# Optimization experiments

Measured on AMD Instinct MI355X. Metric: run time of the kernel, lower is better.

The kernel has to match this reference:

```python
import jax, jax.numpy as jnp
import numpy as np

EPS = 1e-6  # nn.PairwiseDistance default eps (added to the difference)


def setup_inputs() -> dict:
    key = jax.random.key(0)
    feature = jax.random.normal(key, (16384, 256), dtype=jnp.float32)
    return {"feature": feature}


def reference(feature) -> jnp.ndarray:
    n = feature.shape[0]
    # all-pairs inner products [n, n]
    dots = jnp.matmul(feature, feature.T)
    # mask self-similarity on the diagonal with -1 (as in the torch code)
    dots = dots.at[jnp.diag_indices(n)].set(-1.0)
    # row-wise nearest neighbor (argmax of inner product)
    I = jnp.argmax(dots, axis=1)  # [n] int
    # PairwiseDistance(p=2): ||x1 - x2 + eps||_2
    diff = feature - feature[I] + EPS  # [n, d]
    distances = jnp.sqrt(jnp.sum(diff * diff, axis=1))  # [n]
    loss_uniform = -jnp.mean(jnp.log(n * distances))
    return loss_uniform
```

## Files before the change

kernel.cpp:

```cpp
#include <hip/hip_runtime.h>
#include <hip/hip_bf16.h>
#include <math.h>


#define NROWS 16384
#define DIM   256
#define EPSF  1e-6f

typedef __attribute__((ext_vector_type(4))) float f32x4;

typedef const __attribute__((address_space(1))) void* gas1_t;
typedef __attribute__((address_space(3))) void* las3_t;

__device__ __forceinline__ void glds16(const void* g, void* l) {
    __builtin_amdgcn_global_load_lds((gas1_t)g, (las3_t)l, 16, 0, 0);
}

__device__ __forceinline__ unsigned umax2(unsigned a, unsigned b) {
    return a > b ? a : b;
}

__device__ __forceinline__ unsigned f2e4m3(float f) {
    union { float f; unsigned u; } x; x.f = f;
    const unsigned s = (x.u >> 24) & 0x80u;
    const unsigned au = x.u & 0x7FFFFFFFu;
    const float af = __uint_as_float(au);
    if (au < 0x3C800000u) {
        const int q = (int)(af * 512.0f + 0.5f);
        return s | (unsigned)q;
    }
    const unsigned add = 0x7FFFFu + ((au >> 20) & 1u);
    const unsigned v = au + add;
    const unsigned e = (v >> 23) - 120u;
    return s | (e << 3) | ((v >> 20) & 7u);
}

__global__ __launch_bounds__(256)
void convert_kernel(const float* __restrict__ F, unsigned char* __restrict__ F8,
                    unsigned long long* __restrict__ packed)
{
    const int t = blockIdx.x * 256 + threadIdx.x;
    const float4 a = *reinterpret_cast<const float4*>(F + (size_t)t * 8);
    const float4 b = *reinterpret_cast<const float4*>(F + (size_t)t * 8 + 4);
    const unsigned lo = f2e4m3(a.x) | (f2e4m3(a.y) << 8) |
                        (f2e4m3(a.z) << 16) | (f2e4m3(a.w) << 24);
    const unsigned hi = f2e4m3(b.x) | (f2e4m3(b.y) << 8) |
                        (f2e4m3(b.z) << 16) | (f2e4m3(b.w) << 24);
    uint2 v; v.x = lo; v.y = hi;
    *reinterpret_cast<uint2*>(F8 + (size_t)t * 8) = v;
    if (t < NROWS) packed[t] = 0ull;
}

__global__ __launch_bounds__(256, 3)
void mfma_sym_fp8_pipe(const unsigned char* __restrict__ F8,
                       unsigned long long* __restrict__ packed,
                       unsigned long long* __restrict__ scratch)
{
    __shared__ __align__(16) unsigned char As[32768];
    __shared__ __align__(16) unsigned char Bs[16384];
    __shared__ unsigned cmb[256];

    const int tid = threadIdx.x;
    const int w   = tid >> 6;
    const int l   = tid & 63;

    const int bid  = (int)blockIdx.x;
    const int kgen = bid >> 8;
    const int m5   = (bid >> 3) & 31;
    const int ck   = bid & 7;
    const int rs   = (kgen == 0) ? m5 :
                     (kgen == 1) ? 63 - m5 :
                     (kgen == 2) ? 64 + m5 : 127 - m5;
    const int span = 128 - rs;
    const int t0   = rs + ((span * ck) >> 3);
    const int t1   = rs + ((span * (ck + 1)) >> 3);
    if (t0 >= t1) return;

    const int row0 = rs * 128;
    const int wrow = (w >> 1) * 64;
    const int wcol = (w & 1) * 64;
    const int lc   = l & 15;
    const int lr4  = l >> 4;
    const int k16r = lr4 >> 1;
    const int odd  = lr4 & 1;

    #pragma unroll
    for (int m = 0; m < 8; ++m) {
        const int q = 8 * w + m;
        glds16(F8 + (size_t)(row0 + (q & 1) * 64 + l) * DIM + (q >> 1) * 16,
               &As[q * 1024]);
    }
    #pragma unroll
    for (int sl = 0; sl < 3; ++sl)
        glds16(F8 + (size_t)(t0 * 128 + (w & 1) * 64 + l) * DIM + sl * 32 + (w >> 1) * 16,
               &Bs[sl * 4096 + w * 1024]);

    const long* __restrict__ Al = reinterpret_cast<const long*>(As);

    f32x4 acc[4][4];
    #pragma unroll
    for (int i = 0; i < 4; ++i)
        #pragma unroll
        for (int j = 0; j < 4; ++j)
            acc[i][j] = (f32x4){512.f, 512.f, 512.f, 512.f};

    unsigned best[4][4] = {};

    for (int t = t0; t < t1; ++t) {
        const bool dt   = (t == rs);
        const bool last = (t == t1 - 1);

        #pragma unroll
        for (int q = 0; q < 8; ++q) {
            if (!last || q < 6)      asm volatile("s_waitcnt vmcnt(2)" ::: "memory");
            else if (q == 6)         asm volatile("s_waitcnt vmcnt(1)" ::: "memory");
            else                     asm volatile("s_waitcnt vmcnt(0)" ::: "memory");
            __builtin_amdgcn_s_barrier();

            if (!last || q < 5) {
                const int nt = t + ((q + 3) >> 3);
                const int nq = (q + 3) & 7;
                glds16(F8 + (size_t)(nt * 128 + (w & 1) * 64 + l) * DIM
                           + nq * 32 + (w >> 1) * 16,
                       &Bs[((q + 3) & 3) * 4096 + w * 1024]);
            }

            const long* __restrict__ Bl =
                reinterpret_cast<const long*>(Bs + (q & 3) * 4096);

            long afv[4], bfv[4];
            #pragma unroll
            for (int i = 0; i < 4; ++i)
                afv[i] = Al[(2 * q + k16r) * 256 + (wrow + i * 16 + lc) * 2 + odd];
            #pragma unroll
            for (int j = 0; j < 4; ++j)
                bfv[j] = Bl[k16r * 256 + (wcol + j * 16 + lc) * 2 + odd];
            #pragma unroll
            for (int j = 0; j < 4; ++j)
                #pragma unroll
                for (int i = 0; i < 4; ++i)
                    acc[i][j] = __builtin_amdgcn_mfma_f32_16x16x32_fp8_fp8(
                        afv[i], bfv[j], acc[i][j], 0, 0, 0);
        }

        const int tl = t - t0;
        unsigned cbA[4];
        #pragma unroll
        for (int j = 0; j < 4; ++j)
            cbA[j] = 2047u - (unsigned)(tl * 128 + wcol + j * 16 + lc);

        #pragma unroll
        for (int j = 0; j < 4; ++j) {
            unsigned kb = 0u;
            #pragma unroll
            for (int i = 0; i < 4; ++i)
                #pragma unroll
                for (int g = 0; g < 4; ++g) {
                    const int r_loc = wrow + i * 16 + lr4 * 4 + g;
                    unsigned m = __float_as_uint(acc[i][j][g]) & 0xFFFFF800u;
                    if (dt && (wcol + j * 16 + lc == r_loc)) m = 0u;
                    best[i][g] = umax2(best[i][g], m | cbA[j]);
                    kb = umax2(kb, m | (unsigned)(127 - r_loc));
                    acc[i][j][g] = 512.f;
                }
            kb = umax2(kb, (unsigned)__shfl_xor((int)kb, 16));
            kb = umax2(kb, (unsigned)__shfl_xor((int)kb, 32));
            if (lr4 == 0) cmb[(w >> 1) * 128 + wcol + j * 16 + lc] = kb;
        }
        asm volatile("s_waitcnt lgkmcnt(0)" ::: "memory");
        __builtin_amdgcn_s_barrier();
        if (w < 2) {
            const int c = w * 64 + l;
            const unsigned km = umax2(cmb[c], cmb[128 + c]);
            const unsigned grow = (unsigned)row0 + (127u - (km & 0x7FFu));
            scratch[((size_t)t * 128 + rs) * 128 + c] =
                ((unsigned long long)(km & 0xFFFFF800u) << 32) |
                (0xFFFFFFFFu - grow);
        }
    }

    #pragma unroll
    for (int i = 0; i < 4; ++i)
        #pragma unroll
        for (int g = 0; g < 4; ++g) {
            unsigned key = best[i][g];
            #pragma unroll
            for (int m = 8; m >= 1; m >>= 1)
                key = umax2(key, (unsigned)__shfl_xor((int)key, m));
            if (lc == 0) {
                const int r = row0 + wrow + i * 16 + lr4 * 4 + g;
                const unsigned c = (unsigned)(t0 * 128) + (2047u - (key & 0x7FFu));
                atomicMax(&packed[r],
                          ((unsigned long long)(key & 0xFFFFF800u) << 32) |
                          (0xFFFFFFFFu - c));
            }
        }
}

__global__ __launch_bounds__(256)
void dist_loss_kernel(const float* __restrict__ F,
                      const unsigned long long* __restrict__ packed,
                      const unsigned long long* __restrict__ scratch,
                      double* __restrict__ partials)
{
    const int tid  = threadIdx.x;
    const int lane = tid & 63;
    const int w    = tid >> 6;
    const int gw   = blockIdx.x * 4 + w;
    double local = 0.0;
    for (int r = gw; r < NROWS; r += 1024) {
        const int tR = r >> 7;
        const int cl = r & 127;
        unsigned long long best = packed[r];
        const unsigned long long* base = scratch + (size_t)tR * 16384 + cl;
        if (lane <= tR) {
            unsigned long long v = base[(size_t)lane * 128];
            if (lane + 64 <= tR) {
                const unsigned long long v2 = base[(size_t)(lane + 64) * 128];
                if (v2 > v) v = v2;
            }
            if (v > best) best = v;
        }
        #pragma unroll
        for (int m = 32; m >= 1; m >>= 1) {
            const unsigned long long o = __shfl_xor(best, m);
            if (o > best) best = o;
        }
        const int idx = (int)(0xFFFFFFFFu - (unsigned)(best & 0xFFFFFFFFull));

        const float4 a = *reinterpret_cast<const float4*>(
            F + (size_t)r * DIM + (lane << 2));
        const float4 b = *reinterpret_cast<const float4*>(
            F + (size_t)idx * DIM + (lane << 2));
        const float dx = a.x - b.x + EPSF;
        const float dy = a.y - b.y + EPSF;
        const float dz = a.z - b.z + EPSF;
        const float dw = a.w - b.w + EPSF;
        float ss = dx * dx + dy * dy + dz * dz + dw * dw;
        #pragma unroll
        for (int m = 32; m >= 1; m >>= 1) ss += __shfl_xor(ss, m);
        if (lane == 0)
            local += 0.5 * log((double)ss) + log((double)NROWS);
    }
    __shared__ double sm[4];
    if (lane == 0) sm[w] = local;
    __syncthreads();
    if (tid == 0) partials[blockIdx.x] = sm[0] + sm[1] + sm[2] + sm[3];
}

__global__ __launch_bounds__(256)
void finalize_kernel(const double* __restrict__ partials, float* __restrict__ out)
{
    const int tid = threadIdx.x;
    double v = partials[tid];
    #pragma unroll
    for (int m = 32; m >= 1; m >>= 1) v += __shfl_xor(v, m);
    __shared__ double sm[4];
    if ((tid & 63) == 0) sm[tid >> 6] = v;
    __syncthreads();
    if (tid == 0) out[0] = (float)(-(sm[0] + sm[1] + sm[2] + sm[3]) / (double)NROWS);
}

extern "C" void kernel_launch(void* const* d_in, const int* in_sizes, int n_in,
                              void* d_out, int out_size, void* d_ws, size_t ws_size,
                              hipStream_t stream)
{
    const float* F   = (const float*)d_in[0];
    float*       out = (float*)d_out;

    char* ws = (char*)d_ws;
    unsigned char*      F8       = (unsigned char*)ws;
    unsigned long long* packed   = (unsigned long long*)(ws + 4194304);
    unsigned long long* scratch  = (unsigned long long*)(ws + 4325376);
    double*             partials = (double*)(ws + 21102592);

    convert_kernel<<<2048, 256, 0, stream>>>(F, F8, packed);
    mfma_sym_fp8_pipe<<<1024, 256, 0, stream>>>(F8, packed, scratch);
    dist_loss_kernel<<<256, 256, 0, stream>>>(F, packed, scratch, partials);
    finalize_kernel<<<1, 256, 0, stream>>>(partials, out);
}
```

Before: 110.3 us.

## Hold A fragments in registers and double-buffer B tiles in half-K stages

The row-block A fragments now load from LDS into registers once, and the LDS is reused as a two-stage double buffer for B. Each stage covers half of K, so the pipeline goes from an 8-step q loop with hand-tuned vmcnt waits to 2 stages per tile guarded by __syncthreads. The goal is fewer per-step LDS reads of A, fewer barriers and less LDS use (32 KB instead of 48 KB). The change also drops the interleaved block-to-row-strip mapping in favour of a plain linear order, which may hurt load balance over the triangular work. The extra 32 long registers per thread may strain the register budget at 3 waves per SIMD.

```diff
diff --git a/kernel.cpp b/kernel.cpp
--- a/kernel.cpp
+++ b/kernel.cpp
@@ -52,28 +52,21 @@
 }
 
 __global__ __launch_bounds__(256, 3)
-void mfma_sym_fp8_pipe(const unsigned char* __restrict__ F8,
+void mfma_sym_fp8_areg(const unsigned char* __restrict__ F8,
                        unsigned long long* __restrict__ packed,
                        unsigned long long* __restrict__ scratch)
 {
-    __shared__ __align__(16) unsigned char As[32768];
-    __shared__ __align__(16) unsigned char Bs[16384];
+    __shared__ __align__(16) unsigned char Lds[32768];
     __shared__ unsigned cmb[256];
 
     const int tid = threadIdx.x;
     const int w   = tid >> 6;
     const int l   = tid & 63;
-
-    const int bid  = (int)blockIdx.x;
-    const int kgen = bid >> 8;
-    const int m5   = (bid >> 3) & 31;
-    const int ck   = bid & 7;
-    const int rs   = (kgen == 0) ? m5 :
-                     (kgen == 1) ? 63 - m5 :
-                     (kgen == 2) ? 64 + m5 : 127 - m5;
+    const int rs  = (int)blockIdx.x >> 3;
+    const int ck  = (int)blockIdx.x & 7;
     const int span = 128 - rs;
-    const int t0   = rs + ((span * ck) >> 3);
-    const int t1   = rs + ((span * (ck + 1)) >> 3);
+    const int t0  = rs + ((span * ck) >> 3);
+    const int t1  = rs + ((span * (ck + 1)) >> 3);
     if (t0 >= t1) return;
 
     const int row0 = rs * 128;
@@ -88,14 +81,28 @@
     for (int m = 0; m < 8; ++m) {
         const int q = 8 * w + m;
         glds16(F8 + (size_t)(row0 + (q & 1) * 64 + l) * DIM + (q >> 1) * 16,
-               &As[q * 1024]);
-    }
-    #pragma unroll
-    for (int sl = 0; sl < 3; ++sl)
-        glds16(F8 + (size_t)(t0 * 128 + (w & 1) * 64 + l) * DIM + sl * 32 + (w >> 1) * 16,
-               &Bs[sl * 4096 + w * 1024]);
-
-    const long* __restrict__ Al = reinterpret_cast<const long*>(As);
+               &Lds[q * 1024]);
+    }
+    __syncthreads();
+
+    const long* __restrict__ Al = reinterpret_cast<const long*>(Lds);
+    long af[4][8];
+    #pragma unroll
+    for (int i = 0; i < 4; ++i) {
+        const int r2 = (wrow + i * 16 + lc) * 2 + odd;
+        #pragma unroll
+        for (int p = 0; p < 8; ++p)
+            af[i][p] = Al[(p * 2 + k16r) * 256 + r2];
+    }
+    __syncthreads();
+
+    #pragma unroll
+    for (int m = 0; m < 4; ++m) {
+        const int k16 = 2 * w + (m >> 1);
+        const int q2  = m & 1;
+        glds16(F8 + (size_t)(t0 * 128 + q2 * 64 + l) * DIM + k16 * 16,
+               &Lds[k16 * 2048 + q2 * 1024]);
+    }
 
     f32x4 acc[4][4];
     #pragma unroll
@@ -107,40 +114,40 @@
     unsigned best[4][4] = {};
 
     for (int t = t0; t < t1; ++t) {
-        const bool dt   = (t == rs);
-        const bool last = (t == t1 - 1);
-
-        #pragma unroll
-        for (int q = 0; q < 8; ++q) {
-            if (!last || q < 6)      asm volatile("s_waitcnt vmcnt(2)" ::: "memory");
-            else if (q == 6)         asm volatile("s_waitcnt vmcnt(1)" ::: "memory");
-            else                     asm volatile("s_waitcnt vmcnt(0)" ::: "memory");
-            __builtin_amdgcn_s_barrier();
-
-            if (!last || q < 5) {
-                const int nt = t + ((q + 3) >> 3);
-                const int nq = (q + 3) & 7;
-                glds16(F8 + (size_t)(nt * 128 + (w & 1) * 64 + l) * DIM
-                           + nq * 32 + (w >> 1) * 16,
-                       &Bs[((q + 3) & 3) * 4096 + w * 1024]);
+        const bool dt = (t == rs);
+        #pragma unroll
+        for (int ss = 0; ss < 2; ++ss) {
+            __syncthreads();
+
+            const int nt  = ss ? t + 1 : t;
+            const int nss = ss ^ 1;
+            if (nt < t1) {
+                #pragma unroll
+                for (int m = 0; m < 4; ++m) {
+                    const int k16 = 2 * w + (m >> 1);
+                    const int q2  = m & 1;
+                    glds16(F8 + (size_t)(nt * 128 + q2 * 64 + l) * DIM
+                               + nss * 128 + k16 * 16,
+                           &Lds[nss * 16384 + k16 * 2048 + q2 * 1024]);
+                }
             }
 
             const long* __restrict__ Bl =
-                reinterpret_cast<const long*>(Bs + (q & 3) * 4096);
-
-            long afv[4], bfv[4];
+                reinterpret_cast<const long*>(Lds + ss * 16384);
+
             #pragma unroll
-            for (int i = 0; i < 4; ++i)
-                afv[i] = Al[(2 * q + k16r) * 256 + (wrow + i * 16 + lc) * 2 + odd];
-            #pragma unroll
-            for (int j = 0; j < 4; ++j)
-                bfv[j] = Bl[k16r * 256 + (wcol + j * 16 + lc) * 2 + odd];
-            #pragma unroll
-            for (int j = 0; j < 4; ++j)
-                #pragma unroll
-                for (int i = 0; i < 4; ++i)
-                    acc[i][j] = __builtin_amdgcn_mfma_f32_16x16x32_fp8_fp8(
-                        afv[i], bfv[j], acc[i][j], 0, 0, 0);
+            for (int h = 0; h < 4; ++h) {
+                long bfv[4];
+                #pragma unroll
+                for (int j = 0; j < 4; ++j)
+                    bfv[j] = Bl[(h * 2 + k16r) * 256 + (wcol + j * 16 + lc) * 2 + odd];
+                #pragma unroll
+                for (int j = 0; j < 4; ++j)
+                    #pragma unroll
+                    for (int i = 0; i < 4; ++i)
+                        acc[i][j] = __builtin_amdgcn_mfma_f32_16x16x32_fp8_fp8(
+                            af[i][ss * 4 + h], bfv[j], acc[i][j], 0, 0, 0);
+            }
         }
 
         const int tl = t - t0;
@@ -167,8 +174,7 @@
             kb = umax2(kb, (unsigned)__shfl_xor((int)kb, 32));
             if (lr4 == 0) cmb[(w >> 1) * 128 + wcol + j * 16 + lc] = kb;
         }
-        asm volatile("s_waitcnt lgkmcnt(0)" ::: "memory");
-        __builtin_amdgcn_s_barrier();
+        __syncthreads();
         if (w < 2) {
             const int c = w * 64 + l;
             const unsigned km = umax2(cmb[c], cmb[128 + c]);
@@ -275,7 +281,7 @@
     double*             partials = (double*)(ws + 21102592);
 
     convert_kernel<<<2048, 256, 0, stream>>>(F, F8, packed);
-    mfma_sym_fp8_pipe<<<1024, 256, 0, stream>>>(F8, packed, scratch);
+    mfma_sym_fp8_areg<<<1024, 256, 0, stream>>>(F8, packed, scratch);
     dist_loss_kernel<<<256, 256, 0, stream>>>(F, packed, scratch, partials);
     finalize_kernel<<<1, 256, 0, stream>>>(partials, out);
 }
```

Result: slower. 186.5 us (+69.2%).
